# Performance work log

Measured on AMD Instinct MI355X. Metric: run time of the kernel, lower is better.

Reference implementation:

```python
import jax, jax.numpy as jnp
import numpy as np
from jax import lax

B, C, H, W = 16, 256, 56, 56
MID = 16  # SE: max(C//16, 4)
EPS = 1e-5


def _bn(x, g, b, m, v):
    # inference-mode BatchNorm2d folded to per-channel scale/shift
    s = g * lax.rsqrt(v + EPS)
    return x * s[None, :, None, None] + (b - m * s)[None, :, None, None]


def _dw(x, w, ph, pw):
    # depthwise conv, NCHW, kernel w: [C,1,kh,kw]
    return lax.conv_general_dilated(
        x, w, window_strides=(1, 1), padding=[(ph, ph), (pw, pw)],
        dimension_numbers=('NCHW', 'OIHW', 'NCHW'), feature_group_count=C)


def _pw(x, w):
    # 1x1 conv, w: [O,C,1,1]
    return jnp.einsum('bchw,oc->bohw', x, w[:, :, 0, 0])


def _se(x, w1, b1, w2, b2):
    s = x.mean(axis=(2, 3))                      # [B,C] squeeze
    s = jax.nn.relu(s @ w1.T + b1)               # [B,MID]
    s = jax.nn.sigmoid(s @ w2.T + b2)            # [B,C]
    return x * s[:, :, None, None]


def setup_inputs() -> dict:
    key = jax.random.key(0)
    ks = jax.random.split(key, 32)
    rn = lambda i, shape, sc=0.05: jax.random.normal(ks[i], shape, jnp.float32) * sc
    ru = lambda i, shape: jax.random.uniform(ks[i], shape, jnp.float32)
    return {
        'x': rn(0, (B, C, H, W), 1.0),
        'pw1_w': rn(1, (C, C, 1, 1)),
        'xy3_w': rn(2, (C, 1, 3, 3)), 'xy5_w': rn(3, (C, 1, 5, 5)),
        'bnxy_g': ru(4, (C,)), 'bnxy_b': rn(5, (C,)), 'bnxy_m': rn(6, (C,)), 'bnxy_v': ru(7, (C,)),
        'xz3_w': rn(8, (C, 1, 1, 3)), 'xz5_w': rn(9, (C, 1, 1, 5)),
        'bnxz_g': ru(10, (C,)), 'bnxz_b': rn(11, (C,)), 'bnxz_m': rn(12, (C,)), 'bnxz_v': ru(13, (C,)),
        'yz3_w': rn(14, (C, 1, 3, 1)), 'yz5_w': rn(15, (C, 1, 5, 1)),
        'bnyz_g': ru(16, (C,)), 'bnyz_b': rn(17, (C,)), 'bnyz_m': rn(18, (C,)), 'bnyz_v': ru(19, (C,)),
        'alpha': jnp.full((1, C, 1, 1), 0.5, jnp.float32),
        'beta': jnp.full((1, C, 1, 1), 0.5, jnp.float32),
        'pw2_w': rn(20, (C, C, 1, 1)),
        'bn2_g': ru(21, (C,)), 'bn2_b': rn(22, (C,)), 'bn2_m': rn(23, (C,)), 'bn2_v': ru(24, (C,)),
        'fc1_w': rn(25, (MID, C)), 'fc1_b': rn(26, (MID,)),
        'fc2_w': rn(27, (C, MID)), 'fc2_b': rn(28, (C,)),
    }


def reference(x, pw1_w, xy3_w, xy5_w, bnxy_g, bnxy_b, bnxy_m, bnxy_v,
              xz3_w, xz5_w, bnxz_g, bnxz_b, bnxz_m, bnxz_v,
              yz3_w, yz5_w, bnyz_g, bnyz_b, bnyz_m, bnyz_v,
              alpha, beta, pw2_w, bn2_g, bn2_b, bn2_m, bn2_v,
              fc1_w, fc1_b, fc2_w, fc2_b):
    # Pw1: 1x1 conv, no BN / no act
    out = _pw(x, pw1_w)
    # MS_TOP (stride=1 -> pool is identity)
    # [B] xy branch: DW 3x3 + DW 5x5 -> BN -> ReLU
    f_xy = jax.nn.relu(_bn(_dw(out, xy3_w, 1, 1) + _dw(out, xy5_w, 2, 2),
                           bnxy_g, bnxy_b, bnxy_m, bnxy_v))
    # [A] xz branch: per-row depthwise Conv1d along W == depthwise (1,k) 2D conv
    f_xz = jax.nn.relu(_bn(_dw(out, xz3_w, 0, 1) + _dw(out, xz5_w, 0, 2),
                           bnxz_g, bnxz_b, bnxz_m, bnxz_v))
    # [A] yz branch: per-column depthwise Conv1d along H == depthwise (k,1) 2D conv
    f_yz = jax.nn.relu(_bn(_dw(out, yz3_w, 1, 0) + _dw(out, yz5_w, 2, 0),
                           bnyz_g, bnyz_b, bnyz_m, bnyz_v))
    # [C] learnable-gate fusion
    gate = jax.nn.sigmoid(alpha * f_xz + beta * f_yz)
    top = jax.nn.relu(f_xy * gate)
    # Pw2: 1x1 conv -> BN -> ReLU
    out2 = jax.nn.relu(_bn(_pw(top, pw2_w), bn2_g, bn2_b, bn2_m, bn2_v))
    # SE channel attention
    out2 = _se(out2, fc1_w, fc1_b, fc2_w, fc2_b)
    # DropPath is identity at inference; shortcut is identity (stride=1, in==out)
    return out2 + x
```

## Files before the change

### kernel.cpp

```cpp
#include <hip/hip_runtime.h>
#include <math.h>

typedef __bf16 bf16;
typedef __bf16 bf16x8 __attribute__((ext_vector_type(8)));
typedef __bf16 bf16x4 __attribute__((ext_vector_type(4)));
typedef float f32x4 __attribute__((ext_vector_type(4)));

#define CC 256
#define BB 16
#define HH 56
#define WW 56
#define HWSZ 3136
#define EPS 1e-5f

#define OFF_SCALE 0
#define OFF_SUMS  16384
#define OFF_WBF1  32768
#define OFF_WBF2  163840
#define OFF_WDW   294912
#define OFF_BNC   312832
#define OFF_OUT2  321024

__device__ __forceinline__ f32x4 cvt4(bf16x4 v) {
    union { bf16x4 b; unsigned int u[2]; } q; q.b = v;
    f32x4 r;
    r[0] = __uint_as_float(q.u[0] << 16);
    r[1] = __uint_as_float(q.u[0] & 0xffff0000u);
    r[2] = __uint_as_float(q.u[1] << 16);
    r[3] = __uint_as_float(q.u[1] & 0xffff0000u);
    return r;
}

__global__ __launch_bounds__(256) void precast(
    const float* __restrict__ w1, const float* __restrict__ w2,
    const float* __restrict__ xy3, const float* __restrict__ xy5,
    const float* __restrict__ xz3, const float* __restrict__ xz5,
    const float* __restrict__ yz3, const float* __restrict__ yz5,
    const float* __restrict__ gxy, const float* __restrict__ bxy,
    const float* __restrict__ mxy, const float* __restrict__ vxy,
    const float* __restrict__ gxz, const float* __restrict__ bxz,
    const float* __restrict__ mxz, const float* __restrict__ vxz,
    const float* __restrict__ gyz, const float* __restrict__ byz,
    const float* __restrict__ myz, const float* __restrict__ vyz,
    const float* __restrict__ alpha, const float* __restrict__ beta,
    bf16* __restrict__ wbf1, bf16* __restrict__ wbf2,
    bf16* __restrict__ wdw, float* __restrict__ bnc,
    float* __restrict__ sums)
{
    const int blk = blockIdx.x, t = threadIdx.x;
    if (blk < 128) {
        int i = blk * 512 + t * 2;
        wbf1[i] = (bf16)w1[i]; wbf1[i + 1] = (bf16)w1[i + 1];
    } else if (blk < 256) {
        int i = (blk - 128) * 512 + t * 2;
        wbf2[i] = (bf16)w2[i]; wbf2[i + 1] = (bf16)w2[i + 1];
    } else {
        const int c = t;
#pragma unroll
        for (int dh = 0; dh < 5; ++dh)
#pragma unroll
            for (int dw = 0; dw < 5; ++dw) {
                float v = xy5[c * 25 + dh * 5 + dw];
                if (dh >= 1 && dh <= 3 && dw >= 1 && dw <= 3)
                    v += xy3[c * 9 + (dh - 1) * 3 + (dw - 1)];
                wdw[(dh * 5 + dw) * CC + c] = (bf16)v;
            }
#pragma unroll
        for (int d = 0; d < 5; ++d) {
            float v = xz5[c * 5 + d];
            if (d >= 1 && d <= 3) v += xz3[c * 3 + d - 1];
            wdw[(25 + d) * CC + c] = (bf16)v;
            float u = yz5[c * 5 + d];
            if (d >= 1 && d <= 3) u += yz3[c * 3 + d - 1];
            wdw[(30 + d) * CC + c] = (bf16)u;
        }
        float s;
        s = gxy[c] * rsqrtf(vxy[c] + EPS); bnc[0*CC+c] = s; bnc[1*CC+c] = bxy[c] - mxy[c]*s;
        s = gxz[c] * rsqrtf(vxz[c] + EPS); bnc[2*CC+c] = s; bnc[3*CC+c] = bxz[c] - mxz[c]*s;
        s = gyz[c] * rsqrtf(vyz[c] + EPS); bnc[4*CC+c] = s; bnc[5*CC+c] = byz[c] - myz[c]*s;
        bnc[6*CC+c] = alpha[c]; bnc[7*CC+c] = beta[c];
        for (int i = t; i < BB * CC; i += 256) sums[i] = 0.f;
    }
}

__global__ __launch_bounds__(256, 3) void pw_gemm1(
    const float* __restrict__ in, const bf16* __restrict__ wbf,
    bf16* __restrict__ mid)
{
    __shared__ __align__(16) bf16 XT[64][264];
    const int hw0 = blockIdx.x * 64;
    const int b   = blockIdx.y;
    const int t   = threadIdx.x;
    const int lane = t & 63, wv = t >> 6;
    const int q = lane >> 4, n = lane & 15;
    const int co_w = wv * 64;

    bf16x8 aq[4][4];
    const bf16* wp[4];
#pragma unroll
    for (int cf = 0; cf < 4; ++cf) {
        wp[cf] = wbf + (size_t)(co_w + cf * 16 + n) * CC + q * 8;
#pragma unroll
        for (int kx = 0; kx < 4; ++kx)
            aq[cf][kx] = *(const bf16x8*)(wp[cf] + kx * 32);
    }

    {
        const int hwg = (t & 15) * 4;
        const int cig = (t >> 4) * 4;
        const float* base = in + (size_t)b * CC * HWSZ + hw0 + hwg;
#pragma unroll
        for (int pass = 0; pass < 4; ++pass) {
            const int ci0 = pass * 64 + cig;
            f32x4 v[4];
#pragma unroll
            for (int i = 0; i < 4; ++i)
                v[i] = *(const f32x4*)(base + (size_t)(ci0 + i) * HWSZ);
#pragma unroll
            for (int j = 0; j < 4; ++j) {
                bf16x4 r = {(bf16)v[0][j], (bf16)v[1][j], (bf16)v[2][j], (bf16)v[3][j]};
                *(bf16x4*)(&XT[hwg + j][ci0]) = r;
            }
        }
    }
    __syncthreads();

    f32x4 acc[4][4] = {};
#pragma unroll
    for (int half = 0; half < 2; ++half) {
#pragma unroll
        for (int kx = 0; kx < 4; ++kx) {
            const int kk = half * 4 + kx;
            bf16x8 bq[4];
#pragma unroll
            for (int hf = 0; hf < 4; ++hf)
                bq[hf] = *(const bf16x8*)(&XT[hf * 16 + n][kk * 32 + q * 8]);
#pragma unroll
            for (int cf = 0; cf < 4; ++cf)
#pragma unroll
                for (int hf = 0; hf < 4; ++hf)
                    acc[cf][hf] = __builtin_amdgcn_mfma_f32_16x16x32_bf16(
                        aq[cf][kx], bq[hf], acc[cf][hf], 0, 0, 0);
        }
        if (half == 0) {
#pragma unroll
            for (int cf = 0; cf < 4; ++cf)
#pragma unroll
                for (int kx = 0; kx < 4; ++kx)
                    aq[cf][kx] = *(const bf16x8*)(wp[cf] + 128 + kx * 32);
        }
    }

    bf16* ob = mid + ((size_t)b * HWSZ + hw0) * CC;
#pragma unroll
    for (int cf = 0; cf < 4; ++cf) {
        const int co4 = co_w + cf * 16 + q * 4;
#pragma unroll
        for (int hf = 0; hf < 4; ++hf) {
            bf16x4 r = {(bf16)acc[cf][hf][0], (bf16)acc[cf][hf][1],
                        (bf16)acc[cf][hf][2], (bf16)acc[cf][hf][3]};
            *(bf16x4*)(ob + (size_t)(hf * 16 + n) * CC + co4) = r;
        }
    }
}

__global__ __launch_bounds__(256, 2) void dwfuse(
    const bf16* __restrict__ mid, const bf16* __restrict__ wdw,
    const float* __restrict__ bnc, bf16* __restrict__ top)
{
    __shared__ __align__(16) float lwf[35 * 256];
    const int t = threadIdx.x;
    const int lane = t & 63;
    const int wb = blockIdx.x * 8 + (t >> 6) * 2;
    const int h0 = blockIdx.y * 2;
    const size_t plane = (size_t)blockIdx.z * HWSZ;
    const int c0 = lane * 4;
    const bf16* gbase = mid + plane * CC + c0;

    bf16x4 raw[6][6];
#pragma unroll
    for (int r = 0; r < 6; ++r) {
        const int hh = h0 - 2 + r;
        const bool hok = (unsigned)hh < (unsigned)HH;
        const bf16* rp = gbase + (ptrdiff_t)hh * (WW * CC);
#pragma unroll
        for (int wc = 0; wc < 6; ++wc) {
            const int ww = wb - 2 + wc;
            bf16x4 v = {};
            if (hok && (unsigned)ww < (unsigned)WW)
                v = *(const bf16x4*)(rp + (ptrdiff_t)ww * CC);
            raw[r][wc] = v;
        }
    }
    __builtin_amdgcn_sched_barrier(0);

#pragma unroll
    for (int k = 0; k < 35; ++k)
        lwf[k * 256 + t] = (float)wdw[k * 256 + t];
    __syncthreads();

    f32x4 axy[2][2] = {}, axz[2][2] = {}, ayz[2][2] = {};
#pragma unroll
    for (int r = 0; r < 6; ++r) {
        f32x4 fv[6];
#pragma unroll
        for (int wc = 0; wc < 6; ++wc) fv[wc] = cvt4(raw[r][wc]);
#pragma unroll
        for (int ph = 0; ph < 2; ++ph) {
            const int dh = r - ph;
            if (dh < 0 || dh > 4) continue;
#pragma unroll
            for (int dw = 0; dw < 5; ++dw) {
                const f32x4 wt = *(const f32x4*)(&lwf[(dh * 5 + dw) * CC + c0]);
                axy[ph][0] += wt * fv[dw];
                axy[ph][1] += wt * fv[dw + 1];
            }
            if (dh == 2) {
#pragma unroll
                for (int dw = 0; dw < 5; ++dw) {
                    const f32x4 wz = *(const f32x4*)(&lwf[(25 + dw) * CC + c0]);
                    axz[ph][0] += wz * fv[dw];
                    axz[ph][1] += wz * fv[dw + 1];
                }
            }
            {
                const f32x4 wy = *(const f32x4*)(&lwf[(30 + dh) * CC + c0]);
                ayz[ph][0] += wy * fv[2];
                ayz[ph][1] += wy * fv[3];
            }
        }
    }

    const f32x4 sxy = *(const f32x4*)(bnc + 0 * CC + c0);
    const f32x4 hxy = *(const f32x4*)(bnc + 1 * CC + c0);
    const f32x4 sxz = *(const f32x4*)(bnc + 2 * CC + c0);
    const f32x4 hxz = *(const f32x4*)(bnc + 3 * CC + c0);
    const f32x4 syz = *(const f32x4*)(bnc + 4 * CC + c0);
    const f32x4 hyz = *(const f32x4*)(bnc + 5 * CC + c0);
    const f32x4 al  = *(const f32x4*)(bnc + 6 * CC + c0);
    const f32x4 be  = *(const f32x4*)(bnc + 7 * CC + c0);

#pragma unroll
    for (int ph = 0; ph < 2; ++ph)
#pragma unroll
        for (int pw = 0; pw < 2; ++pw) {
            const f32x4 txy = axy[ph][pw] * sxy + hxy;
            const f32x4 txz = axz[ph][pw] * sxz + hxz;
            const f32x4 tyz = ayz[ph][pw] * syz + hyz;
            bf16x4 rr;
#pragma unroll
            for (int j = 0; j < 4; ++j) {
                const float fxy = fmaxf(txy[j], 0.f);
                const float fxz = fmaxf(txz[j], 0.f);
                const float fyz = fmaxf(tyz[j], 0.f);
                const float z   = al[j] * fxz + be[j] * fyz;
                const float g   = 1.f / (1.f + __expf(-z));
                rr[j] = (bf16)(fxy * g);
            }
            *(bf16x4*)(top + (plane + (size_t)(h0 + ph) * WW + (wb + pw)) * CC + c0) = rr;
        }
}

__global__ __launch_bounds__(256, 3) void pw_gemm2(
    const bf16* __restrict__ top, const bf16* __restrict__ wbf,
    const float* __restrict__ g2, const float* __restrict__ b2,
    const float* __restrict__ m2, const float* __restrict__ v2,
    bf16* __restrict__ out2, float* __restrict__ sums)
{
    __shared__ __align__(16) bf16 XT[64][264];
    const int hw0 = blockIdx.x * 64;
    const int b   = blockIdx.y;
    const int t   = threadIdx.x;
    const int lane = t & 63, wv = t >> 6;
    const int q = lane >> 4, n = lane & 15;
    const int co_w = wv * 64;

    bf16x8 aq[4][4];
    const bf16* wp[4];
#pragma unroll
    for (int cf = 0; cf < 4; ++cf) {
        wp[cf] = wbf + (size_t)(co_w + cf * 16 + n) * CC + q * 8;
#pragma unroll
        for (int kx = 0; kx < 4; ++kx)
            aq[cf][kx] = *(const bf16x8*)(wp[cf] + kx * 32);
    }

    {
        const int hw_r = t >> 2;
        const int k0   = (t & 3) * 64;
        const bf16* src = top + ((size_t)b * HWSZ + hw0 + hw_r) * CC + k0;
#pragma unroll
        for (int j = 0; j < 8; ++j)
            *(bf16x8*)(&XT[hw_r][k0 + j * 8]) = *(const bf16x8*)(src + j * 8);
    }
    __syncthreads();

    f32x4 acc[4][4] = {};
#pragma unroll
    for (int half = 0; half < 2; ++half) {
#pragma unroll
        for (int kx = 0; kx < 4; ++kx) {
            const int kk = half * 4 + kx;
            bf16x8 bq[4];
#pragma unroll
            for (int hf = 0; hf < 4; ++hf)
                bq[hf] = *(const bf16x8*)(&XT[hf * 16 + n][kk * 32 + q * 8]);
#pragma unroll
            for (int cf = 0; cf < 4; ++cf)
#pragma unroll
                for (int hf = 0; hf < 4; ++hf)
                    acc[cf][hf] = __builtin_amdgcn_mfma_f32_16x16x32_bf16(
                        aq[cf][kx], bq[hf], acc[cf][hf], 0, 0, 0);
        }
        if (half == 0) {
#pragma unroll
            for (int cf = 0; cf < 4; ++cf)
#pragma unroll
                for (int kx = 0; kx < 4; ++kx)
                    aq[cf][kx] = *(const bf16x8*)(wp[cf] + 128 + kx * 32);
        }
    }

    bf16* ob = out2 + ((size_t)b * HWSZ + hw0) * CC;
#pragma unroll
    for (int cf = 0; cf < 4; ++cf) {
        const int co4 = co_w + cf * 16 + q * 4;
        f32x4 g = *(const f32x4*)(g2 + co4);
        f32x4 bb = *(const f32x4*)(b2 + co4);
        f32x4 mm = *(const f32x4*)(m2 + co4);
        f32x4 vv = *(const f32x4*)(v2 + co4);
        f32x4 sc, sh;
#pragma unroll
        for (int r = 0; r < 4; ++r) {
            sc[r] = g[r] * rsqrtf(vv[r] + EPS);
            sh[r] = bb[r] - mm[r] * sc[r];
        }
        f32x4 rs = {};
#pragma unroll
        for (int hf = 0; hf < 4; ++hf) {
            bf16x4 r4;
#pragma unroll
            for (int r = 0; r < 4; ++r) {
                float v = fmaxf(acc[cf][hf][r] * sc[r] + sh[r], 0.f);
                rs[r] += v;
                r4[r] = (bf16)v;
            }
            *(bf16x4*)(ob + (size_t)(hf * 16 + n) * CC + co4) = r4;
        }
#pragma unroll
        for (int msk = 1; msk < 16; msk <<= 1)
#pragma unroll
            for (int r = 0; r < 4; ++r) rs[r] += __shfl_xor(rs[r], msk);
        if (n == 0) {
#pragma unroll
            for (int r = 0; r < 4; ++r)
                atomicAdd(&sums[b * CC + co4 + r], rs[r]);
        }
    }
}

__global__ __launch_bounds__(256) void se_apply(
    const bf16* __restrict__ out2, const float* __restrict__ x,
    const float* __restrict__ sums,
    const float* __restrict__ w1, const float* __restrict__ b1,
    const float* __restrict__ w2, const float* __restrict__ b2,
    float* __restrict__ out)
{
    __shared__ float TT[64 * 68];
    __shared__ float mean[256];
    __shared__ float hid[16];
    __shared__ __align__(16) float scl[64];
    const int hw0 = blockIdx.x * 64;
    const int c0  = blockIdx.y * 64;
    const int b   = blockIdx.z;
    const int t   = threadIdx.x;

    mean[t] = sums[b * CC + t] * (1.f / (float)HWSZ);
    __syncthreads();
    {
        const int m = t >> 4, l = t & 15;
        const float* wr = w1 + m * CC + l * 16;
        const float* mr = mean + l * 16;
        float h = 0.f;
#pragma unroll
        for (int j = 0; j < 16; ++j) h += wr[j] * mr[j];
#pragma unroll
        for (int msk = 1; msk < 16; msk <<= 1) h += __shfl_xor(h, msk);
        if (l == 0) hid[m] = fmaxf(h + b1[m], 0.f);
    }
    __syncthreads();
    if (t < 64) {
        const int c = c0 + t;
        float v = b2[c];
#pragma unroll
        for (int md = 0; md < 16; ++md) v += w2[c * 16 + md] * hid[md];
        scl[t] = 1.f / (1.f + __expf(-v));
    }
    __syncthreads();

    {
        const int hw_r = t >> 2;
        const int coff = (t & 3) * 16;
        const bf16* p = out2 + ((size_t)b * HWSZ + hw0 + hw_r) * CC + c0 + coff;
        bf16x8 u0 = *(const bf16x8*)(p);
        bf16x8 u1 = *(const bf16x8*)(p + 8);
        f32x4 s0 = *(const f32x4*)(&scl[coff]);
        f32x4 s1 = *(const f32x4*)(&scl[coff + 4]);
        f32x4 s2 = *(const f32x4*)(&scl[coff + 8]);
        f32x4 s3 = *(const f32x4*)(&scl[coff + 12]);
#pragma unroll
        for (int j = 0; j < 4; ++j) {
            TT[(coff + j)      * 68 + hw_r] = (float)u0[j]     * s0[j];
            TT[(coff + 4 + j)  * 68 + hw_r] = (float)u0[4 + j] * s1[j];
            TT[(coff + 8 + j)  * 68 + hw_r] = (float)u1[j]     * s2[j];
            TT[(coff + 12 + j) * 68 + hw_r] = (float)u1[4 + j] * s3[j];
        }
    }
    __syncthreads();
    {
        const int c_r   = t >> 2;
        const int hwoff = (t & 3) * 16;
        const size_t go = ((size_t)b * CC + c0 + c_r) * HWSZ + hw0 + hwoff;
#pragma unroll
        for (int v = 0; v < 4; ++v) {
            f32x4 tv = *(const f32x4*)(&TT[c_r * 68 + hwoff + v * 4]);
            f32x4 xv = *(const f32x4*)(x + go + v * 4);
#pragma unroll
            for (int j = 0; j < 4; ++j) tv[j] += xv[j];
            *(f32x4*)(out + go + v * 4) = tv;
        }
    }
}

extern "C" void kernel_launch(void* const* d_in, const int* in_sizes, int n_in,
                              void* d_out, int out_size, void* d_ws, size_t ws_size,
                              hipStream_t stream)
{
    const float* x      = (const float*)d_in[0];
    const float* pw1_w  = (const float*)d_in[1];
    const float* xy3_w  = (const float*)d_in[2];
    const float* xy5_w  = (const float*)d_in[3];
    const float* bnxy_g = (const float*)d_in[4];
    const float* bnxy_b = (const float*)d_in[5];
    const float* bnxy_m = (const float*)d_in[6];
    const float* bnxy_v = (const float*)d_in[7];
    const float* xz3_w  = (const float*)d_in[8];
    const float* xz5_w  = (const float*)d_in[9];
    const float* bnxz_g = (const float*)d_in[10];
    const float* bnxz_b = (const float*)d_in[11];
    const float* bnxz_m = (const float*)d_in[12];
    const float* bnxz_v = (const float*)d_in[13];
    const float* yz3_w  = (const float*)d_in[14];
    const float* yz5_w  = (const float*)d_in[15];
    const float* bnyz_g = (const float*)d_in[16];
    const float* bnyz_b = (const float*)d_in[17];
    const float* bnyz_m = (const float*)d_in[18];
    const float* bnyz_v = (const float*)d_in[19];
    const float* alpha  = (const float*)d_in[20];
    const float* beta   = (const float*)d_in[21];
    const float* pw2_w  = (const float*)d_in[22];
    const float* bn2_g  = (const float*)d_in[23];
    const float* bn2_b  = (const float*)d_in[24];
    const float* bn2_m  = (const float*)d_in[25];
    const float* bn2_v  = (const float*)d_in[26];
    const float* fc1_w  = (const float*)d_in[27];
    const float* fc1_b  = (const float*)d_in[28];
    const float* fc2_w  = (const float*)d_in[29];
    const float* fc2_b  = (const float*)d_in[30];

    const size_t NEL = (size_t)BB * CC * HWSZ;
    char* ws = (char*)d_ws;
    float* sums  = (float*)(ws + OFF_SUMS);
    bf16*  wbf1  = (bf16*) (ws + OFF_WBF1);
    bf16*  wbf2  = (bf16*) (ws + OFF_WBF2);
    bf16*  wdw   = (bf16*) (ws + OFF_WDW);
    float* bnc   = (float*)(ws + OFF_BNC);
    bf16*  out2  = (bf16*) (ws + OFF_OUT2);
    bf16*  mid   = (bf16*)d_out;
    bf16*  top   = (bf16*)d_out + NEL;

    precast<<<257, 256, 0, stream>>>(pw1_w, pw2_w,
        xy3_w, xy5_w, xz3_w, xz5_w, yz3_w, yz5_w,
        bnxy_g, bnxy_b, bnxy_m, bnxy_v,
        bnxz_g, bnxz_b, bnxz_m, bnxz_v,
        bnyz_g, bnyz_b, bnyz_m, bnyz_v,
        alpha, beta, wbf1, wbf2, wdw, bnc, sums);

    pw_gemm1<<<dim3(49, 16), 256, 0, stream>>>(x, wbf1, mid);
    dwfuse<<<dim3(7, 28, 16), 256, 0, stream>>>(mid, wdw, bnc, top);
    pw_gemm2<<<dim3(49, 16), 256, 0, stream>>>(top, wbf2, bn2_g, bn2_b,
                                               bn2_m, bn2_v, out2, sums);
    se_apply<<<dim3(49, 4, 16), 256, 0, stream>>>(out2, x, sums,
        fc1_w, fc1_b, fc2_w, fc2_b, (float*)d_out);
}
```

Measured before the change: 262.3 us.

## Fuse depthwise stage into second pointwise GEMM via shared-memory tile

Merges the depthwise/gate kernel with the second 1x1 conv GEMM: each block writes its 16 gated pixels into an LDS tile and immediately runs the MFMA GEMM, BN, ReLU and SE-sum on them. This removes the global write and re-read of the intermediate top tensor and one kernel launch. In exchange each block reloads the full pw2 weight matrix for only 16 pixels and issues four times more atomic adds for the SE sums, raising L2 traffic and atomic contention.

Measured after the change: 328.2 us. 1.25x slower.

```diff
diff --git a/kernel.cpp b/kernel.cpp
--- a/kernel.cpp
+++ b/kernel.cpp
@@ -164,16 +164,23 @@
     }
 }
 
-__global__ __launch_bounds__(256, 2) void dwfuse(
+__global__ __launch_bounds__(256, 2) void dw_gemm2(
     const bf16* __restrict__ mid, const bf16* __restrict__ wdw,
-    const float* __restrict__ bnc, bf16* __restrict__ top)
+    const float* __restrict__ bnc, const bf16* __restrict__ wbf,
+    const float* __restrict__ g2, const float* __restrict__ b2,
+    const float* __restrict__ m2, const float* __restrict__ v2,
+    bf16* __restrict__ out2, float* __restrict__ sums)
 {
     __shared__ __align__(16) float lwf[35 * 256];
+    __shared__ __align__(16) bf16 XT[16][264];
     const int t = threadIdx.x;
     const int lane = t & 63;
-    const int wb = blockIdx.x * 8 + (t >> 6) * 2;
+    const int wv = t >> 6;
+    const int wb0 = blockIdx.x * 8;
+    const int wb = wb0 + wv * 2;
     const int h0 = blockIdx.y * 2;
-    const size_t plane = (size_t)blockIdx.z * HWSZ;
+    const int b  = blockIdx.z;
+    const size_t plane = (size_t)b * HWSZ;
     const int c0 = lane * 4;
     const bf16* gbase = mid + plane * CC + c0;
 
@@ -231,47 +238,37 @@
         }
     }
 
-    const f32x4 sxy = *(const f32x4*)(bnc + 0 * CC + c0);
-    const f32x4 hxy = *(const f32x4*)(bnc + 1 * CC + c0);
-    const f32x4 sxz = *(const f32x4*)(bnc + 2 * CC + c0);
-    const f32x4 hxz = *(const f32x4*)(bnc + 3 * CC + c0);
-    const f32x4 syz = *(const f32x4*)(bnc + 4 * CC + c0);
-    const f32x4 hyz = *(const f32x4*)(bnc + 5 * CC + c0);
-    const f32x4 al  = *(const f32x4*)(bnc + 6 * CC + c0);
-    const f32x4 be  = *(const f32x4*)(bnc + 7 * CC + c0);
-
-#pragma unroll
-    for (int ph = 0; ph < 2; ++ph)
-#pragma unroll
-        for (int pw = 0; pw < 2; ++pw) {
-            const f32x4 txy = axy[ph][pw] * sxy + hxy;
-            const f32x4 txz = axz[ph][pw] * sxz + hxz;
-            const f32x4 tyz = ayz[ph][pw] * syz + hyz;
-            bf16x4 rr;
-#pragma unroll
-            for (int j = 0; j < 4; ++j) {
-                const float fxy = fmaxf(txy[j], 0.f);
-                const float fxz = fmaxf(txz[j], 0.f);
-                const float fyz = fmaxf(tyz[j], 0.f);
-                const float z   = al[j] * fxz + be[j] * fyz;
-                const float g   = 1.f / (1.f + __expf(-z));
-                rr[j] = (bf16)(fxy * g);
-            }
-            *(bf16x4*)(top + (plane + (size_t)(h0 + ph) * WW + (wb + pw)) * CC + c0) = rr;
-        }
-}
-
-__global__ __launch_bounds__(256, 3) void pw_gemm2(
-    const bf16* __restrict__ top, const bf16* __restrict__ wbf,
-    const float* __restrict__ g2, const float* __restrict__ b2,
-    const float* __restrict__ m2, const float* __restrict__ v2,
-    bf16* __restrict__ out2, float* __restrict__ sums)
-{
-    __shared__ __align__(16) bf16 XT[64][264];
-    const int hw0 = blockIdx.x * 64;
-    const int b   = blockIdx.y;
-    const int t   = threadIdx.x;
-    const int lane = t & 63, wv = t >> 6;
+    {
+        const f32x4 sxy = *(const f32x4*)(bnc + 0 * CC + c0);
+        const f32x4 hxy = *(const f32x4*)(bnc + 1 * CC + c0);
+        const f32x4 sxz = *(const f32x4*)(bnc + 2 * CC + c0);
+        const f32x4 hxz = *(const f32x4*)(bnc + 3 * CC + c0);
+        const f32x4 syz = *(const f32x4*)(bnc + 4 * CC + c0);
+        const f32x4 hyz = *(const f32x4*)(bnc + 5 * CC + c0);
+        const f32x4 al  = *(const f32x4*)(bnc + 6 * CC + c0);
+        const f32x4 be  = *(const f32x4*)(bnc + 7 * CC + c0);
+#pragma unroll
+        for (int ph = 0; ph < 2; ++ph)
+#pragma unroll
+            for (int pw = 0; pw < 2; ++pw) {
+                const f32x4 txy = axy[ph][pw] * sxy + hxy;
+                const f32x4 txz = axz[ph][pw] * sxz + hxz;
+                const f32x4 tyz = ayz[ph][pw] * syz + hyz;
+                bf16x4 rr;
+#pragma unroll
+                for (int j = 0; j < 4; ++j) {
+                    const float fxy = fmaxf(txy[j], 0.f);
+                    const float fxz = fmaxf(txz[j], 0.f);
+                    const float fyz = fmaxf(tyz[j], 0.f);
+                    const float z   = al[j] * fxz + be[j] * fyz;
+                    const float g   = 1.f / (1.f + __expf(-z));
+                    rr[j] = (bf16)(fxy * g);
+                }
+                *(bf16x4*)(&XT[ph * 8 + wv * 2 + pw][c0]) = rr;
+            }
+    }
+    __syncthreads();
+
     const int q = lane >> 4, n = lane & 15;
     const int co_w = wv * 64;
 
@@ -285,32 +282,17 @@
             aq[cf][kx] = *(const bf16x8*)(wp[cf] + kx * 32);
     }
 
-    {
-        const int hw_r = t >> 2;
-        const int k0   = (t & 3) * 64;
-        const bf16* src = top + ((size_t)b * HWSZ + hw0 + hw_r) * CC + k0;
-#pragma unroll
-        for (int j = 0; j < 8; ++j)
-            *(bf16x8*)(&XT[hw_r][k0 + j * 8]) = *(const bf16x8*)(src + j * 8);
-    }
-    __syncthreads();
-
-    f32x4 acc[4][4] = {};
+    f32x4 acc[4] = {};
 #pragma unroll
     for (int half = 0; half < 2; ++half) {
 #pragma unroll
         for (int kx = 0; kx < 4; ++kx) {
             const int kk = half * 4 + kx;
-            bf16x8 bq[4];
-#pragma unroll
-            for (int hf = 0; hf < 4; ++hf)
-                bq[hf] = *(const bf16x8*)(&XT[hf * 16 + n][kk * 32 + q * 8]);
+            const bf16x8 bq = *(const bf16x8*)(&XT[n][kk * 32 + q * 8]);
 #pragma unroll
             for (int cf = 0; cf < 4; ++cf)
-#pragma unroll
-                for (int hf = 0; hf < 4; ++hf)
-                    acc[cf][hf] = __builtin_amdgcn_mfma_f32_16x16x32_bf16(
-                        aq[cf][kx], bq[hf], acc[cf][hf], 0, 0, 0);
+                acc[cf] = __builtin_amdgcn_mfma_f32_16x16x32_bf16(
+                    aq[cf][kx], bq, acc[cf], 0, 0, 0);
         }
         if (half == 0) {
 #pragma unroll
@@ -321,7 +303,7 @@
         }
     }
 
-    bf16* ob = out2 + ((size_t)b * HWSZ + hw0) * CC;
+    bf16* ob = out2 + (plane + (size_t)(h0 + (n >> 3)) * WW + wb0 + (n & 7)) * CC;
 #pragma unroll
     for (int cf = 0; cf < 4; ++cf) {
         const int co4 = co_w + cf * 16 + q * 4;
@@ -335,18 +317,15 @@
             sc[r] = g[r] * rsqrtf(vv[r] + EPS);
             sh[r] = bb[r] - mm[r] * sc[r];
         }
-        f32x4 rs = {};
-#pragma unroll
-        for (int hf = 0; hf < 4; ++hf) {
-            bf16x4 r4;
-#pragma unroll
-            for (int r = 0; r < 4; ++r) {
-                float v = fmaxf(acc[cf][hf][r] * sc[r] + sh[r], 0.f);
-                rs[r] += v;
-                r4[r] = (bf16)v;
-            }
-            *(bf16x4*)(ob + (size_t)(hf * 16 + n) * CC + co4) = r4;
-        }
+        f32x4 rs;
+        bf16x4 r4;
+#pragma unroll
+        for (int r = 0; r < 4; ++r) {
+            float v = fmaxf(acc[cf][r] * sc[r] + sh[r], 0.f);
+            rs[r] = v;
+            r4[r] = (bf16)v;
+        }
+        *(bf16x4*)(ob + co4) = r4;
 #pragma unroll
         for (int msk = 1; msk < 16; msk <<= 1)
 #pragma unroll
@@ -477,7 +456,6 @@
     float* bnc   = (float*)(ws + OFF_BNC);
     bf16*  out2  = (bf16*) (ws + OFF_OUT2);
     bf16*  mid   = (bf16*)d_out;
-    bf16*  top   = (bf16*)d_out + NEL;
 
     precast<<<257, 256, 0, stream>>>(pw1_w, pw2_w,
         xy3_w, xy5_w, xz3_w, xz5_w, yz3_w, yz5_w,
@@ -487,9 +465,9 @@
         alpha, beta, wbf1, wbf2, wdw, bnc, sums);
 
     pw_gemm1<<<dim3(49, 16), 256, 0, stream>>>(x, wbf1, mid);
-    dwfuse<<<dim3(7, 28, 16), 256, 0, stream>>>(mid, wdw, bnc, top);
-    pw_gemm2<<<dim3(49, 16), 256, 0, stream>>>(top, wbf2, bn2_g, bn2_b,
-                                               bn2_m, bn2_v, out2, sums);
+    dw_gemm2<<<dim3(7, 28, 16), 256, 0, stream>>>(mid, wdw, bnc, wbf2,
+                                                  bn2_g, bn2_b, bn2_m, bn2_v,
+                                                  out2, sums);
     se_apply<<<dim3(49, 4, 16), 256, 0, stream>>>(out2, x, sums,
         fc1_w, fc1_b, fc2_w, fc2_b, (float*)d_out);
 }
```
